# Optimization experiments

Measured on AMD Instinct MI355X. Metric: run time of the kernel, lower is better.

Reference implementation:

```python
import jax, jax.numpy as jnp
import numpy as np

PAD = 0  # dictionary.word2idx['<pad>']
H, D, L1, L2, B = 4, 128, 512, 512, 64
W_SCALE = 1.0 / np.sqrt(D)


def setup_inputs() -> dict:
    key = jax.random.key(0)
    k1, k2, k3, k4, k5, k6 = jax.random.split(key, 6)
    return {
        "input1": jax.random.normal(k1, (L1, B, D), dtype=jnp.float32),
        "input2": jax.random.normal(k2, (L2, B, D), dtype=jnp.float32),
        "raw1": jax.random.randint(k3, (L1, B), 0, 50, dtype=jnp.int64),
        "raw2": jax.random.randint(k4, (L2, B), 0, 50, dtype=jnp.int64),
        "W_U": jax.random.normal(k5, (H, D, D), dtype=jnp.float32) * W_SCALE,
        "W_ipm": jax.random.normal(k6, (D, D), dtype=jnp.float32) * W_SCALE,
    }


def reference(input1, input2, raw1, raw2, W_U, W_ipm):
    # input1: [L1,B,D], input2: [L2,B,D] (seq-first, as in the torch module)
    dt = input1.dtype
    mask1 = (raw1 == PAD).astype(dt).T  # [B,L1]
    mask2 = (raw2 == PAD).astype(dt).T  # [B,L2]

    # All hops batched: G[b,h,l,m] = tanh( x1[l,b,:] . (W_U[h] @ x2[m,b,:]) )
    G = jnp.tanh(jnp.einsum('lbd,hde,mbe->bhlm', input1, W_U, input2))  # [B,H,L1,L2]

    # masked max-reduce then softmax over the remaining sequence axis
    s1 = jnp.max(G - 10000.0 * mask2[:, None, None, :], axis=3)  # [B,H,L1]
    s2 = jnp.max(G - 10000.0 * mask1[:, None, :, None], axis=2)  # [B,H,L2]
    a1 = jax.nn.softmax(s1, axis=2)  # [B,H,L1]
    a2 = jax.nn.softmax(s2, axis=2)  # [B,H,L2]

    # weighted read-out
    r1 = jnp.einsum('bhl,lbd->bhd', a1, input1)  # [B,H,D]
    r2 = jnp.einsum('bhm,mbd->bhd', a2, input2)  # [B,H,D]

    # combine_hops: adist = softmax(tanh(sum(r1 * IPM(r2), -1)), over hops)
    ipm_r2 = jnp.einsum('bhe,de->bhd', r2, W_ipm)
    adist = jax.nn.softmax(jnp.tanh(jnp.sum(r1 * ipm_r2, axis=2)), axis=1)  # [B,H]
    r1f = jnp.einsum('bh,bhd->bd', adist, r1)  # [B,D]
    r2f = jnp.einsum('bh,bhd->bd', adist, r2)  # [B,D]
    return (r1f, r2f, a1, a2, adist)
```

## Files before the change

### kernel.cpp

```cpp
#include <hip/hip_runtime.h>

#define Bn 64
#define Dn 128
#define Ln 512

typedef __attribute__((ext_vector_type(8))) _Float16 half8;
typedef __attribute__((ext_vector_type(4))) float f32x4;

__device__ __forceinline__ void split8h(const float* xs, half8& hi, half8& lo) {
#pragma unroll
  for (int j = 0; j < 8; ++j) {
    _Float16 h = (_Float16)xs[j];
    hi[j] = h;
    lo[j] = (_Float16)(xs[j] - (float)h);
  }
}
__device__ __forceinline__ void cvt8h(const float* xs, half8& hi) {
#pragma unroll
  for (int j = 0; j < 8; ++j) hi[j] = (_Float16)xs[j];
}
__device__ __forceinline__ void gll16(const void* g, void* l) {
  __builtin_amdgcn_global_load_lds(
      (const __attribute__((address_space(1))) void*)g,
      (__attribute__((address_space(3))) void*)l, 16, 0, 0);
}

__global__ __launch_bounds__(256) void kw(const float* __restrict__ WU,
                                          _Float16* __restrict__ wimg) {
  int blk = blockIdx.x;
  int t = threadIdx.x, ln = t & 63, ks = t >> 6;
  int h = blk >> 3, dgrp = blk & 7;
  int d = dgrp * 16 + (ln & 15), e = ks * 32 + (ln >> 4) * 8;
  const float* src = WU + ((size_t)h * Dn + d) * Dn + e;
  float xs[8];
  *(float4*)xs = *(const float4*)src;
  *(float4*)(xs + 4) = *(const float4*)(src + 4);
  half8 hi;
  cvt8h(xs, hi);
  size_t u = (size_t)((h * 8 + dgrp) * 4 + ks) * 512 + (size_t)ln * 8;
  *(half8*)(wimg + u) = hi;
}

__global__ __launch_bounds__(256, 3) void kz(const float* __restrict__ X2,
                                             const _Float16* __restrict__ wimg,
                                             _Float16* __restrict__ zimg) {
  __shared__ __align__(16) float zt[64 * 132];
  int orig = blockIdx.x;
  int blk = (orig & 7) * 256 + (orig >> 3);
  int h = blk & 3, mt6 = (blk >> 2) & 7, b = blk >> 5;
  int t = threadIdx.x, ln = t & 63, wv = t >> 6;
  int rg = wv >> 1, cb = wv & 1;
  int R0 = rg * 32;
  int eo = (ln >> 4) * 8;

  half8 ahf[2][4], alf[2][4];
#pragma unroll
  for (int mr = 0; mr < 2; ++mr) {
    const float* rsrc =
        X2 + ((size_t)(mt6 * 64 + R0 + mr * 16 + (ln & 15)) * Bn + b) * Dn + eo;
#pragma unroll
    for (int ks = 0; ks < 4; ++ks) {
      float xs[8];
      *(float4*)xs = *(const float4*)(rsrc + ks * 32);
      *(float4*)(xs + 4) = *(const float4*)(rsrc + ks * 32 + 4);
      split8h(xs, ahf[mr][ks], alf[mr][ks]);
    }
  }

  const f32x4 fz = {0.f, 0.f, 0.f, 0.f};
#pragma unroll
  for (int ph = 0; ph < 2; ++ph) {
    f32x4 acc[2][2];
#pragma unroll
    for (int i = 0; i < 2; ++i) {
      acc[i][0] = fz;
      acc[i][1] = fz;
    }
    int dg0 = cb * 4 + ph * 2;
#pragma unroll
    for (int ks = 0; ks < 4; ++ks) {
      const _Float16* ub =
          wimg + (size_t)((h * 8 + dg0) * 4 + ks) * 512 + (size_t)ln * 8;
      half8 b0 = *(const half8*)ub;
      half8 b1 = *(const half8*)(ub + 2048);
#pragma unroll
      for (int mr = 0; mr < 2; ++mr) {
        acc[mr][0] = __builtin_amdgcn_mfma_f32_16x16x32_f16(ahf[mr][ks], b0, acc[mr][0], 0, 0, 0);
        acc[mr][0] = __builtin_amdgcn_mfma_f32_16x16x32_f16(alf[mr][ks], b0, acc[mr][0], 0, 0, 0);
        acc[mr][1] = __builtin_amdgcn_mfma_f32_16x16x32_f16(ahf[mr][ks], b1, acc[mr][1], 0, 0, 0);
        acc[mr][1] = __builtin_amdgcn_mfma_f32_16x16x32_f16(alf[mr][ks], b1, acc[mr][1], 0, 0, 0);
      }
    }
#pragma unroll
    for (int mr = 0; mr < 2; ++mr) {
      int rb = R0 + mr * 16 + (ln >> 4) * 4;
#pragma unroll
      for (int nr = 0; nr < 2; ++nr) {
        int d = cb * 64 + ph * 32 + nr * 16 + (ln & 15);
#pragma unroll
        for (int j = 0; j < 4; ++j) zt[(rb + j) * 132 + d] = acc[mr][nr][j];
      }
    }
  }
  __syncthreads();
  int bh = b * 4 + h;
#pragma unroll
  for (int p = 0; p < 4; ++p) {
    int u = p * 4 + wv;
    int r = (u >> 2) * 16 + (ln & 15);
    int d = (u & 3) * 32 + eo;
    float xs[8];
    *(float4*)xs = *(const float4*)(zt + r * 132 + d);
    *(float4*)(xs + 4) = *(const float4*)(zt + r * 132 + d + 4);
    half8 hi;
    cvt8h(xs, hi);
    size_t ub = (((size_t)bh * 32 + mt6 * 4 + (u >> 2)) * 4 + (u & 3)) * 512 +
                (size_t)ln * 8;
    *(half8*)(zimg + ub) = hi;
  }
}

__global__ __launch_bounds__(256, 2) void k1(const float* __restrict__ X1,
                                             const _Float16* __restrict__ zimg,
                                             const int* __restrict__ raw1,
                                             const int* __restrict__ raw2,
                                             float* __restrict__ s1,
                                             float* __restrict__ s2pp) {
  __shared__ __align__(16) char Bbuf[2][16384];
  __shared__ float m1f[256];
  __shared__ float m2f[512];
  __shared__ float cmbuf[4][512];

  int orig = blockIdx.x;
  int blk = (orig & 7) * 64 + (orig >> 3);
  int rh = blk & 1, h = (blk >> 1) & 3, b = blk >> 3;
  int bh = b * 4 + h;
  int t = threadIdx.x, ln = t & 63, wv = t >> 6;
  int R0 = rh * 256 + wv * 64;

  m1f[t] = (raw1[(size_t)(rh * 256 + t) * Bn + b] == 0) ? 1.0e4f : 0.0f;
  for (int i = t; i < 512; i += 256)
    m2f[i] = (raw2[(size_t)i * Bn + b] == 0) ? 1.0e4f : 0.0f;

#define STAGE(bb, c_)                                                    \
  {                                                                      \
    size_t ub = ((size_t)bh * 32 + (c_)*4) * 2048;                       \
    _Pragma("unroll") for (int p = 0; p < 4; ++p) {                      \
      gll16(zimg + ub + (size_t)(wv + p * 4) * 512 + (size_t)ln * 8,     \
            Bbuf[bb] + (wv + p * 4) * 1024);                             \
    }                                                                    \
  }

  STAGE(0, 0);

  half8 ahf[4][4];
  {
    int eo = (ln >> 4) * 8;
#pragma unroll
    for (int mr = 0; mr < 4; ++mr) {
      const float* rsrc =
          X1 + ((size_t)(R0 + mr * 16 + (ln & 15)) * Bn + b) * Dn + eo;
#pragma unroll
      for (int ks = 0; ks < 4; ++ks) {
        float xs[8];
        *(float4*)xs = *(const float4*)(rsrc + ks * 32);
        *(float4*)(xs + 4) = *(const float4*)(rsrc + ks * 32 + 4);
        cvt8h(xs, ahf[mr][ks]);
      }
    }
  }
  __syncthreads();

  float msub1[4][4];
#pragma unroll
  for (int mr = 0; mr < 4; ++mr)
#pragma unroll
    for (int j = 0; j < 4; ++j)
      msub1[mr][j] = m1f[wv * 64 + mr * 16 + (ln >> 4) * 4 + j];

  float rmrun[4][4];
#pragma unroll
  for (int i = 0; i < 4; ++i)
#pragma unroll
    for (int j = 0; j < 4; ++j) rmrun[i][j] = -3.0e38f;

  const f32x4 fz = {0.f, 0.f, 0.f, 0.f};
  int cur = 0;
  for (int c = 0; c < 8; ++c) {
    if (c < 7) STAGE(cur ^ 1, c + 1);

    f32x4 acc[4][4];
#pragma unroll
    for (int i = 0; i < 4; ++i)
#pragma unroll
      for (int n = 0; n < 4; ++n) acc[i][n] = fz;
#pragma unroll
    for (int ks = 0; ks < 4; ++ks) {
      const char* base = Bbuf[cur] + ks * 1024 + ln * 16;
      half8 b0 = *(const half8*)base;
      half8 b1 = *(const half8*)(base + 4096);
      half8 b2 = *(const half8*)(base + 8192);
      half8 b3 = *(const half8*)(base + 12288);
#pragma unroll
      for (int mr = 0; mr < 4; ++mr) {
        acc[mr][0] = __builtin_amdgcn_mfma_f32_16x16x32_f16(ahf[mr][ks], b0, acc[mr][0], 0, 0, 0);
        acc[mr][1] = __builtin_amdgcn_mfma_f32_16x16x32_f16(ahf[mr][ks], b1, acc[mr][1], 0, 0, 0);
        acc[mr][2] = __builtin_amdgcn_mfma_f32_16x16x32_f16(ahf[mr][ks], b2, acc[mr][2], 0, 0, 0);
        acc[mr][3] = __builtin_amdgcn_mfma_f32_16x16x32_f16(ahf[mr][ks], b3, acc[mr][3], 0, 0, 0);
      }
    }
    float ms[4];
#pragma unroll
    for (int nr = 0; nr < 4; ++nr) ms[nr] = m2f[c * 64 + nr * 16 + (ln & 15)];
#pragma unroll
    for (int mr = 0; mr < 4; ++mr)
#pragma unroll
      for (int j = 0; j < 4; ++j) {
        float cc = fmaxf(fmaxf(acc[mr][0][j] - ms[0], acc[mr][1][j] - ms[1]),
                         fmaxf(acc[mr][2][j] - ms[2], acc[mr][3][j] - ms[3]));
        rmrun[mr][j] = fmaxf(rmrun[mr][j], cc);
      }
#pragma unroll
    for (int nr = 0; nr < 4; ++nr) {
      float v = -3.0e38f;
#pragma unroll
      for (int mr = 0; mr < 4; ++mr)
#pragma unroll
        for (int j = 0; j < 4; ++j) v = fmaxf(v, acc[mr][nr][j] - msub1[mr][j]);
      v = fmaxf(v, __shfl_xor(v, 16));
      v = fmaxf(v, __shfl_xor(v, 32));
      if (ln < 16) cmbuf[wv][c * 64 + nr * 16 + ln] = v;
    }
    __syncthreads();
    cur ^= 1;
  }
#undef STAGE

#pragma unroll
  for (int off = 1; off < 16; off <<= 1)
#pragma unroll
    for (int mr = 0; mr < 4; ++mr)
#pragma unroll
      for (int j = 0; j < 4; ++j)
        rmrun[mr][j] = fmaxf(rmrun[mr][j], __shfl_xor(rmrun[mr][j], off));
  if ((ln & 15) == 0) {
    float* dst = s1 + (size_t)bh * 512 + R0 + (ln >> 4) * 4;
#pragma unroll
    for (int mr = 0; mr < 4; ++mr)
#pragma unroll
      for (int j = 0; j < 4; ++j) dst[mr * 16 + j] = rmrun[mr][j];
  }
  for (int i = t; i < 512; i += 256) {
    float v = fmaxf(fmaxf(cmbuf[0][i], cmbuf[1][i]),
                    fmaxf(cmbuf[2][i], cmbuf[3][i]));
    s2pp[((size_t)bh * 2 + rh) * 512 + i] = v;
  }
}

__global__ __launch_bounds__(256) void k2(const float* __restrict__ s1,
                                          const float* __restrict__ s2pp,
                                          const float* __restrict__ X1,
                                          const float* __restrict__ X2,
                                          float* __restrict__ out,
                                          float* __restrict__ rws4) {
  __shared__ float aL[4][512];
  __shared__ f32x4 redv[4][8][32];
  int blk = blockIdx.x;
  int side = blk >> 8, b = (blk >> 2) & 63, lq = blk & 3;
  int t = threadIdx.x, ln = t & 63, h = t >> 6;
  int bh = b * 4 + h;
  int base = ln * 8;

  float vals[8];
  if (side == 0) {
    const float* p = s1 + (size_t)bh * 512 + base;
    float4 va = *(const float4*)p;
    float4 vb = *(const float4*)(p + 4);
    vals[0] = va.x; vals[1] = va.y; vals[2] = va.z; vals[3] = va.w;
    vals[4] = vb.x; vals[5] = vb.y; vals[6] = vb.z; vals[7] = vb.w;
  } else {
    const float* p0 = s2pp + (size_t)bh * 1024 + base;
    float4 va0 = *(const float4*)p0;
    float4 va1 = *(const float4*)(p0 + 4);
    float4 vb0 = *(const float4*)(p0 + 512);
    float4 vb1 = *(const float4*)(p0 + 516);
    vals[0] = fmaxf(va0.x, vb0.x); vals[1] = fmaxf(va0.y, vb0.y);
    vals[2] = fmaxf(va0.z, vb0.z); vals[3] = fmaxf(va0.w, vb0.w);
    vals[4] = fmaxf(va1.x, vb1.x); vals[5] = fmaxf(va1.y, vb1.y);
    vals[6] = fmaxf(va1.z, vb1.z); vals[7] = fmaxf(va1.w, vb1.w);
  }
#pragma unroll
  for (int q = 0; q < 8; ++q) vals[q] = tanhf(vals[q]);
  float mx = vals[0];
#pragma unroll
  for (int q = 1; q < 8; ++q) mx = fmaxf(mx, vals[q]);
#pragma unroll
  for (int off = 1; off < 64; off <<= 1) mx = fmaxf(mx, __shfl_xor(mx, off));
  float s = 0.0f;
#pragma unroll
  for (int q = 0; q < 8; ++q) {
    vals[q] = expf(vals[q] - mx);
    s += vals[q];
  }
#pragma unroll
  for (int off = 1; off < 64; off <<= 1) s += __shfl_xor(s, off);
  float inv = 1.0f / s;
#pragma unroll
  for (int q = 0; q < 8; ++q) vals[q] *= inv;

  if (lq == 0) {
    int aoff = (side == 0 ? 16384 : 147456) + bh * 512 + base;
    *(float4*)(out + aoff) = make_float4(vals[0], vals[1], vals[2], vals[3]);
    *(float4*)(out + aoff + 4) = make_float4(vals[4], vals[5], vals[6], vals[7]);
  }
  *(float4*)(&aL[h][base]) = make_float4(vals[0], vals[1], vals[2], vals[3]);
  *(float4*)(&aL[h][base + 4]) = make_float4(vals[4], vals[5], vals[6], vals[7]);
  __syncthreads();

  const float4* X4 = (const float4*)(side == 0 ? X1 : X2);
  int q = t & 31, lg = t >> 5;
  f32x4 av[4];
  const f32x4 fz = {0.f, 0.f, 0.f, 0.f};
#pragma unroll
  for (int hh = 0; hh < 4; ++hh) av[hh] = fz;
#pragma unroll 4
  for (int l = lq * 128 + lg; l < lq * 128 + 128; l += 8) {
    float4 xv = X4[((size_t)l * Bn + b) * 32 + q];
#pragma unroll
    for (int hh = 0; hh < 4; ++hh) {
      float w = aL[hh][l];
      av[hh][0] += w * xv.x;
      av[hh][1] += w * xv.y;
      av[hh][2] += w * xv.z;
      av[hh][3] += w * xv.w;
    }
  }
#pragma unroll
  for (int hh = 0; hh < 4; ++hh) redv[hh][lg][q] = av[hh];
  __syncthreads();
  if (t < 128) {
    int d = t;
#pragma unroll
    for (int hh = 0; hh < 4; ++hh) {
      float s2v = 0.0f;
#pragma unroll
      for (int g = 0; g < 8; ++g) s2v += ((const float*)&redv[hh][g][d >> 2])[d & 3];
      rws4[(((size_t)(side * 64 + b) * 4 + hh) * 4 + lq) * 128 + d] = s2v;
    }
  }
}

__global__ __launch_bounds__(128) void k3(const float* __restrict__ rws4,
                                          const float* __restrict__ Wipm,
                                          float* __restrict__ out) {
  int b = blockIdx.x, t = threadIdx.x;
  __shared__ float r2l[4][128];
  __shared__ float tsum[2][4];
  float r1h[4], r2h[4];
#pragma unroll
  for (int h = 0; h < 4; ++h) {
    float a0 = 0.f, a1 = 0.f;
#pragma unroll
    for (int lq = 0; lq < 4; ++lq) {
      a0 += rws4[(((size_t)b * 4 + h) * 4 + lq) * 128 + t];
      a1 += rws4[(((size_t)(64 + b) * 4 + h) * 4 + lq) * 128 + t];
    }
    r1h[h] = a0;
    r2h[h] = a1;
    r2l[h][t] = a1;
  }
  __syncthreads();
  float p[4] = {0, 0, 0, 0};
  for (int e = 0; e < 128; ++e) {
    float w = Wipm[t * 128 + e];
#pragma unroll
    for (int h = 0; h < 4; ++h) p[h] += w * r2l[h][e];
  }
#pragma unroll
  for (int h = 0; h < 4; ++h) p[h] *= r1h[h];
#pragma unroll
  for (int off = 1; off < 64; off <<= 1)
#pragma unroll
    for (int h = 0; h < 4; ++h) p[h] += __shfl_xor(p[h], off);
  if ((t & 63) == 0)
#pragma unroll
    for (int h = 0; h < 4; ++h) tsum[t >> 6][h] = p[h];
  __syncthreads();
  float ad[4], mx = -3.0e38f;
#pragma unroll
  for (int h = 0; h < 4; ++h) {
    float v = tanhf(tsum[0][h] + tsum[1][h]);
    ad[h] = v;
    mx = fmaxf(mx, v);
  }
  float s = 0.0f;
#pragma unroll
  for (int h = 0; h < 4; ++h) { ad[h] = expf(ad[h] - mx); s += ad[h]; }
  float inv = 1.0f / s;
#pragma unroll
  for (int h = 0; h < 4; ++h) ad[h] *= inv;
  if (t < 4) out[278528 + b * 4 + t] = ad[t];
  float f1 = 0.0f, f2 = 0.0f;
#pragma unroll
  for (int h = 0; h < 4; ++h) { f1 += ad[h] * r1h[h]; f2 += ad[h] * r2h[h]; }
  out[b * 128 + t] = f1;
  out[8192 + b * 128 + t] = f2;
}

extern "C" void kernel_launch(void* const* d_in, const int* in_sizes, int n_in,
                              void* d_out, int out_size, void* d_ws,
                              size_t ws_size, hipStream_t stream) {
  (void)in_sizes; (void)n_in; (void)out_size; (void)ws_size;
  const float* x1 = (const float*)d_in[0];
  const float* x2 = (const float*)d_in[1];
  const int* raw1 = (const int*)d_in[2];
  const int* raw2 = (const int*)d_in[3];
  const float* wu = (const float*)d_in[4];
  const float* wipm = (const float*)d_in[5];
  float* out = (float*)d_out;
  char* w = (char*)d_ws;
  _Float16* zimg = (_Float16*)w;
  _Float16* wimg = (_Float16*)(w + 67108864);
  float* s1 = (float*)(w + 67633152);
  float* s2pp = (float*)(w + 68157440);
  float* rws4 = (float*)(w + 69206016);

  kw<<<32, 256, 0, stream>>>(wu, wimg);
  kz<<<2048, 256, 0, stream>>>(x2, wimg, zimg);
  k1<<<512, 256, 0, stream>>>(x1, zimg, raw1, raw2, s1, s2pp);
  k2<<<512, 256, 0, stream>>>(s1, s2pp, x1, x2, out, rws4);
  k3<<<64, 128, 0, stream>>>(rws4, wipm, out);
}
```

Measured before the change: 79.43 us.

## Drop fp16 lo-split for X2 and fuse W_U conversion into kz

Removes the hi/lo fp16 split of input2 in the Z = W_U·x2 projection, which halves the MFMA count there, and drops the separate kw kernel that pre-converted W_U to fp16. kz now reads W_U in fp32 directly and converts it in registers. This saves one kernel launch and half the projection MFMAs, at the cost of lower precision in Z and redundant fp32 W_U reads across the 2048 blocks.

Result: slower. 95.03 us (+19.6%).

```diff
diff --git a/kernel.cpp b/kernel.cpp
--- a/kernel.cpp
+++ b/kernel.cpp
@@ -7,14 +7,6 @@
 typedef __attribute__((ext_vector_type(8))) _Float16 half8;
 typedef __attribute__((ext_vector_type(4))) float f32x4;
 
-__device__ __forceinline__ void split8h(const float* xs, half8& hi, half8& lo) {
-#pragma unroll
-  for (int j = 0; j < 8; ++j) {
-    _Float16 h = (_Float16)xs[j];
-    hi[j] = h;
-    lo[j] = (_Float16)(xs[j] - (float)h);
-  }
-}
 __device__ __forceinline__ void cvt8h(const float* xs, half8& hi) {
 #pragma unroll
   for (int j = 0; j < 8; ++j) hi[j] = (_Float16)xs[j];
@@ -25,24 +17,8 @@
       (__attribute__((address_space(3))) void*)l, 16, 0, 0);
 }
 
-__global__ __launch_bounds__(256) void kw(const float* __restrict__ WU,
-                                          _Float16* __restrict__ wimg) {
-  int blk = blockIdx.x;
-  int t = threadIdx.x, ln = t & 63, ks = t >> 6;
-  int h = blk >> 3, dgrp = blk & 7;
-  int d = dgrp * 16 + (ln & 15), e = ks * 32 + (ln >> 4) * 8;
-  const float* src = WU + ((size_t)h * Dn + d) * Dn + e;
-  float xs[8];
-  *(float4*)xs = *(const float4*)src;
-  *(float4*)(xs + 4) = *(const float4*)(src + 4);
-  half8 hi;
-  cvt8h(xs, hi);
-  size_t u = (size_t)((h * 8 + dgrp) * 4 + ks) * 512 + (size_t)ln * 8;
-  *(half8*)(wimg + u) = hi;
-}
-
 __global__ __launch_bounds__(256, 3) void kz(const float* __restrict__ X2,
-                                             const _Float16* __restrict__ wimg,
+                                             const float* __restrict__ WU,
                                              _Float16* __restrict__ zimg) {
   __shared__ __align__(16) float zt[64 * 132];
   int orig = blockIdx.x;
@@ -53,7 +29,7 @@
   int R0 = rg * 32;
   int eo = (ln >> 4) * 8;
 
-  half8 ahf[2][4], alf[2][4];
+  half8 ahf[2][4];
 #pragma unroll
   for (int mr = 0; mr < 2; ++mr) {
     const float* rsrc =
@@ -63,34 +39,39 @@
       float xs[8];
       *(float4*)xs = *(const float4*)(rsrc + ks * 32);
       *(float4*)(xs + 4) = *(const float4*)(rsrc + ks * 32 + 4);
-      split8h(xs, ahf[mr][ks], alf[mr][ks]);
+      cvt8h(xs, ahf[mr][ks]);
     }
   }
 
   const f32x4 fz = {0.f, 0.f, 0.f, 0.f};
 #pragma unroll
   for (int ph = 0; ph < 2; ++ph) {
+    half8 bhf[2][4];
+#pragma unroll
+    for (int nr = 0; nr < 2; ++nr) {
+      int d = cb * 64 + ph * 32 + nr * 16 + (ln & 15);
+      const float* wsrc = WU + ((size_t)h * Dn + d) * Dn + eo;
+#pragma unroll
+      for (int ks = 0; ks < 4; ++ks) {
+        float xs[8];
+        *(float4*)xs = *(const float4*)(wsrc + ks * 32);
+        *(float4*)(xs + 4) = *(const float4*)(wsrc + ks * 32 + 4);
+        cvt8h(xs, bhf[nr][ks]);
+      }
+    }
     f32x4 acc[2][2];
 #pragma unroll
     for (int i = 0; i < 2; ++i) {
       acc[i][0] = fz;
       acc[i][1] = fz;
     }
-    int dg0 = cb * 4 + ph * 2;
-#pragma unroll
-    for (int ks = 0; ks < 4; ++ks) {
-      const _Float16* ub =
-          wimg + (size_t)((h * 8 + dg0) * 4 + ks) * 512 + (size_t)ln * 8;
-      half8 b0 = *(const half8*)ub;
-      half8 b1 = *(const half8*)(ub + 2048);
+#pragma unroll
+    for (int ks = 0; ks < 4; ++ks)
 #pragma unroll
       for (int mr = 0; mr < 2; ++mr) {
-        acc[mr][0] = __builtin_amdgcn_mfma_f32_16x16x32_f16(ahf[mr][ks], b0, acc[mr][0], 0, 0, 0);
-        acc[mr][0] = __builtin_amdgcn_mfma_f32_16x16x32_f16(alf[mr][ks], b0, acc[mr][0], 0, 0, 0);
-        acc[mr][1] = __builtin_amdgcn_mfma_f32_16x16x32_f16(ahf[mr][ks], b1, acc[mr][1], 0, 0, 0);
-        acc[mr][1] = __builtin_amdgcn_mfma_f32_16x16x32_f16(alf[mr][ks], b1, acc[mr][1], 0, 0, 0);
-      }
-    }
+        acc[mr][0] = __builtin_amdgcn_mfma_f32_16x16x32_f16(ahf[mr][ks], bhf[0][ks], acc[mr][0], 0, 0, 0);
+        acc[mr][1] = __builtin_amdgcn_mfma_f32_16x16x32_f16(ahf[mr][ks], bhf[1][ks], acc[mr][1], 0, 0, 0);
+      }
 #pragma unroll
     for (int mr = 0; mr < 2; ++mr) {
       int rb = R0 + mr * 16 + (ln >> 4) * 4;
@@ -420,13 +401,11 @@
   float* out = (float*)d_out;
   char* w = (char*)d_ws;
   _Float16* zimg = (_Float16*)w;
-  _Float16* wimg = (_Float16*)(w + 67108864);
   float* s1 = (float*)(w + 67633152);
   float* s2pp = (float*)(w + 68157440);
   float* rws4 = (float*)(w + 69206016);
 
-  kw<<<32, 256, 0, stream>>>(wu, wimg);
-  kz<<<2048, 256, 0, stream>>>(x2, wimg, zimg);
+  kz<<<2048, 256, 0, stream>>>(x2, wu, zimg);
   k1<<<512, 256, 0, stream>>>(x1, zimg, raw1, raw2, s1, s2pp);
   k2<<<512, 256, 0, stream>>>(s1, s2pp, x1, x2, out, rws4);
   k3<<<64, 128, 0, stream>>>(rws4, wipm, out);
```
